# Performance work log

Measured on AMD Instinct MI355X. Metric: run time of the kernel, lower is better.

## Reference

```python
import jax, jax.numpy as jnp
import numpy as np

HEADS = 4
OUT_CH = 32
IN_CH = 128
HC = HEADS * OUT_CH  # 128
N = 100000
G = 1000
E = 1600000
EG = 16000
NEG_SLOPE = 0.2


def gat_conv(x, edge_index, W, att_src, att_dst, bias):
    """PyG-style GATConv (concat heads, self-loops, leaky_relu 0.2, eval mode)."""
    n = x.shape[0]
    loop = jnp.arange(n)
    src = jnp.concatenate([edge_index[0], loop])
    dst = jnp.concatenate([edge_index[1], loop])
    h = (x @ W).reshape(n, HEADS, OUT_CH)            # [n,H,C]
    a_src = (h * att_src).sum(-1)                    # [n,H]
    a_dst = (h * att_dst).sum(-1)                    # [n,H]
    e = jax.nn.leaky_relu(a_src[src] + a_dst[dst], NEG_SLOPE)  # [e,H]
    m = jax.ops.segment_max(e, dst, num_segments=n)
    ex = jnp.exp(e - m[dst])
    s = jax.ops.segment_sum(ex, dst, num_segments=n)
    alpha = ex / (s[dst] + 1e-16)
    out = jax.ops.segment_sum(alpha[:, :, None] * h[src], dst, num_segments=n)
    return out.reshape(n, HC) + bias


def setup_inputs() -> dict:
    key = jax.random.key(0)
    ks = jax.random.split(key, 16)
    inv = 1.0 / np.sqrt(IN_CH)
    invh = 1.0 / np.sqrt(HC)
    return {
        "x": jax.random.normal(ks[0], (N, IN_CH), jnp.float32),
        "x_g": jax.random.normal(ks[1], (G, IN_CH), jnp.float32),
        "edge_index": jax.random.randint(ks[2], (2, E), 0, N, jnp.int32),
        "edge_index_g": jax.random.randint(ks[3], (2, EG), 0, G, jnp.int32),
        "node_group": jax.random.randint(ks[4], (N,), 0, G, jnp.int32),
        "W1": jax.random.normal(ks[5], (IN_CH, HC), jnp.float32) * inv,
        "att_src1": jax.random.normal(ks[6], (HEADS, OUT_CH), jnp.float32) * invh,
        "att_dst1": jax.random.normal(ks[7], (HEADS, OUT_CH), jnp.float32) * invh,
        "bias1": jnp.zeros((HC,), jnp.float32),
        "W2": jax.random.normal(ks[8], (IN_CH, HC), jnp.float32) * inv,
        "att_src2": jax.random.normal(ks[9], (HEADS, OUT_CH), jnp.float32) * invh,
        "att_dst2": jax.random.normal(ks[10], (HEADS, OUT_CH), jnp.float32) * invh,
        "bias2": jnp.zeros((HC,), jnp.float32),
        "W_fc": jax.random.normal(ks[11], (HC, OUT_CH), jnp.float32) * invh,
        "b_fc": jnp.zeros((OUT_CH,), jnp.float32),
    }


def reference(x, x_g, edge_index, edge_index_g, node_group,
              W1, att_src1, att_dst1, bias1,
              W2, att_src2, att_dst2, bias2, W_fc, b_fc):
    x_out = gat_conv(x, edge_index, W1, att_src1, att_dst1, bias1)      # [N,HC]
    x_g_out = gat_conv(x_g, edge_index_g, W2, att_src2, att_dst2, bias2)  # [G,HC]

    # mean of adjacent group features per group (segment mean over group edges)
    adj_sum = jax.ops.segment_sum(x_g_out[edge_index_g[1]], edge_index_g[0], num_segments=G)
    cnt = jax.ops.segment_sum(jnp.ones((edge_index_g.shape[1],), x_g_out.dtype),
                              edge_index_g[0], num_segments=G)
    adj_mean = adj_sum / jnp.maximum(cnt, 1.0)[:, None]                  # [G,HC]

    gf = x_g_out[node_group]          # per-node own-group feature   [N,HC]
    af = adj_mean[node_group]         # per-node adjacent-group mean [N,HC]
    imp_g = jnp.einsum('nc,nc->n', x_out, gf)
    imp_a = jnp.einsum('nc,nc->n', x_out, af)
    upd = x_out + imp_g[:, None] * gf + imp_a[:, None] * af
    out = upd @ W_fc + b_fc
    return out, x_g_out
```

## Files before the change

### kernel.cpp

```cpp
#include <hip/hip_runtime.h>

__host__ __device__ static inline int imin(int a, int b) { return a < b ? a : b; }

__device__ __forceinline__ float lrelu(float v) { return v > 0.f ? v : 0.2f * v; }

__global__ __launch_bounds__(256) void gemm128(const float* __restrict__ X,
                                               const float* __restrict__ W,
                                               const float* __restrict__ att_s,
                                               const float* __restrict__ att_d,
                                               float* __restrict__ H,
                                               float* __restrict__ asrc,
                                               float* __restrict__ adst, int n) {
  __shared__ float Wl[128 * 128];
  __shared__ float Xl[4][4 * 128];
  const int tid = threadIdx.x;
  for (int i = tid; i < 4096; i += 256)
    ((float4*)Wl)[i] = ((const float4*)W)[i];
  __syncthreads();

  const int wave = tid >> 6, lane = tid & 63;
  const float as_l = att_s[lane], as_h = att_s[lane + 64];
  const float ad_l = att_d[lane], ad_h = att_d[lane + 64];
  const int nb = (n + 15) >> 4;
  for (int tb = blockIdx.x; tb < nb; tb += gridDim.x) {
    const int rbase = tb * 16 + wave * 4;
    float2* xl2 = (float2*)&Xl[wave][0];
#pragma unroll
    for (int rr = 0; rr < 4; ++rr) {
      int r = rbase + rr;
      float2 v = make_float2(0.f, 0.f);
      if (r < n) v = ((const float2*)(X + (size_t)r * 128))[lane];
      xl2[rr * 64 + lane] = v;
    }
    float a0[4] = {0, 0, 0, 0}, a1[4] = {0, 0, 0, 0};
#pragma unroll 4
    for (int c = 0; c < 128; ++c) {
      float w0 = Wl[c * 128 + lane];
      float w1 = Wl[c * 128 + lane + 64];
#pragma unroll
      for (int rr = 0; rr < 4; ++rr) {
        float xc = Xl[wave][rr * 128 + c];
        a0[rr] = fmaf(xc, w0, a0[rr]);
        a1[rr] = fmaf(xc, w1, a1[rr]);
      }
    }
#pragma unroll
    for (int rr = 0; rr < 4; ++rr) {
      int r = rbase + rr;
      if (r < n) {
        H[(size_t)r * 128 + lane] = a0[rr];
        H[(size_t)r * 128 + lane + 64] = a1[rr];
        float ps0 = a0[rr] * as_l, pd0 = a0[rr] * ad_l;
        float ps1 = a1[rr] * as_h, pd1 = a1[rr] * ad_h;
#pragma unroll
        for (int m = 16; m >= 1; m >>= 1) {
          ps0 += __shfl_xor(ps0, m);
          pd0 += __shfl_xor(pd0, m);
          ps1 += __shfl_xor(ps1, m);
          pd1 += __shfl_xor(pd1, m);
        }
        if (lane == 0) {
          asrc[(size_t)r * 4 + 0] = ps0;
          adst[(size_t)r * 4 + 0] = pd0;
          asrc[(size_t)r * 4 + 2] = ps1;
          adst[(size_t)r * 4 + 2] = pd1;
        } else if (lane == 32) {
          asrc[(size_t)r * 4 + 1] = ps0;
          adst[(size_t)r * 4 + 1] = pd0;
          asrc[(size_t)r * 4 + 3] = ps1;
          adst[(size_t)r * 4 + 3] = pd1;
        }
      }
    }
  }
}

__global__ __launch_bounds__(256) void count_deg(const int* __restrict__ dst, int ne,
                                                 int* __restrict__ deg) {
  int i = blockIdx.x * 256 + threadIdx.x;
  if (i < ne) atomicAdd(&deg[dst[i]], 1);
}

__global__ __launch_bounds__(256) void scan_part1(const int* __restrict__ in, int n,
                                                  int* __restrict__ bsum) {
  int base = blockIdx.x * 4096 + threadIdx.x * 16;
  int s = 0;
  if (base + 16 <= n) {
    const int4* p = (const int4*)(in + base);
#pragma unroll
    for (int k = 0; k < 4; ++k) {
      int4 v = p[k];
      s += v.x + v.y + v.z + v.w;
    }
  } else {
    for (int k = 0; k < 16; ++k) {
      int i = base + k;
      if (i < n) s += in[i];
    }
  }
#pragma unroll
  for (int o = 1; o < 64; o <<= 1) s += __shfl_xor(s, o);
  __shared__ int ws[4];
  int wave = threadIdx.x >> 6, lane = threadIdx.x & 63;
  if (lane == 0) ws[wave] = s;
  __syncthreads();
  if (threadIdx.x == 0) bsum[blockIdx.x] = ws[0] + ws[1] + ws[2] + ws[3];
}

__global__ __launch_bounds__(256) void scan_part2(int* __restrict__ bsum, int nb,
                                                  int* __restrict__ off, int n) {
  __shared__ int sm[256];
  int tid = threadIdx.x;
  int v = (tid < nb) ? bsum[tid] : 0;
  sm[tid] = v;
  __syncthreads();
  int x = v;
  for (int o = 1; o < 256; o <<= 1) {
    int t = (tid >= o) ? sm[tid - o] : 0;
    __syncthreads();
    x += t;
    sm[tid] = x;
    __syncthreads();
  }
  if (tid < nb) bsum[tid] = x - v;
  if (tid == 0) off[n] = sm[255];
}

__global__ __launch_bounds__(256) void scan_part3(const int* __restrict__ in, int n,
                                                  const int* __restrict__ bsum,
                                                  int* __restrict__ out) {
  int tid = threadIdx.x;
  int base = blockIdx.x * 4096 + tid * 16;
  int vals[16];
  if (base + 16 <= n) {
    const int4* p = (const int4*)(in + base);
#pragma unroll
    for (int k = 0; k < 4; ++k) {
      int4 v = p[k];
      vals[4 * k] = v.x;
      vals[4 * k + 1] = v.y;
      vals[4 * k + 2] = v.z;
      vals[4 * k + 3] = v.w;
    }
  } else {
#pragma unroll
    for (int k = 0; k < 16; ++k) {
      int i = base + k;
      vals[k] = (i < n) ? in[i] : 0;
    }
  }
  int tsum = 0;
#pragma unroll
  for (int k = 0; k < 16; ++k) tsum += vals[k];
  int lane = tid & 63, wave = tid >> 6;
  int inc = tsum;
#pragma unroll
  for (int o = 1; o < 64; o <<= 1) {
    int t = __shfl_up(inc, o);
    if (lane >= o) inc += t;
  }
  int exc = inc - tsum;
  __shared__ int ws[4];
  if (lane == 63) ws[wave] = inc;
  __syncthreads();
  int woff = 0;
  for (int w = 0; w < wave; ++w) woff += ws[w];
  int off0 = bsum[blockIdx.x] + woff + exc;
  int run = 0;
#pragma unroll
  for (int k = 0; k < 16; ++k) {
    int i = base + k;
    if (i < n) out[i] = off0 + run;
    run += vals[k];
  }
}

__global__ __launch_bounds__(256) void fill_csr(const int* __restrict__ src,
                                                const int* __restrict__ dst, int ne,
                                                const int* __restrict__ off,
                                                int* __restrict__ cur,
                                                int* __restrict__ csr) {
  int i = blockIdx.x * 256 + threadIdx.x;
  if (i < ne) {
    int d = dst[i];
    int p = atomicAdd(&cur[d], 1);
    csr[off[d] + p] = src[i];
  }
}

__global__ __launch_bounds__(256) void gat_aggregate(
    const float* __restrict__ H, const float* __restrict__ asrc,
    const float* __restrict__ adst, const int* __restrict__ off,
    const int* __restrict__ csr, const float* __restrict__ bias,
    float* __restrict__ out, int n) {
  __shared__ float4 exl[4][64];
  int gw = (blockIdx.x * 256 + threadIdx.x) >> 6;
  if (gw >= n) return;
  int wave = (threadIdx.x >> 6), lane = threadIdx.x & 63;
  int n0 = off[gw];
  int deg = off[gw + 1] - n0;

  float4 ad = ((const float4*)adst)[gw];
  int c0 = lane * 2;
  int hd = lane >> 4;
  float4 s4 = make_float4(0.f, 0.f, 0.f, 0.f);
  float acc0 = 0.f, acc1 = 0.f;
  const float* exw = (const float*)&exl[wave][0];

  for (int base = 0; base < deg; base += 64) {
    int idx = base + lane;
    bool v = idx < deg;
    int sr = v ? csr[n0 + idx] : 0;
    float4 ex = make_float4(0.f, 0.f, 0.f, 0.f);
    if (v) {
      float4 as = ((const float4*)asrc)[sr];
      ex.x = __expf(lrelu(as.x + ad.x));
      ex.y = __expf(lrelu(as.y + ad.y));
      ex.z = __expf(lrelu(as.z + ad.z));
      ex.w = __expf(lrelu(as.w + ad.w));
      s4.x += ex.x;
      s4.y += ex.y;
      s4.z += ex.z;
      s4.w += ex.w;
    }
    exl[wave][lane] = ex;
    int cnt = imin(64, deg - base);
    for (int j = 0; j < cnt; ++j) {
      int srj = __shfl(sr, j);
      float exh = exw[j * 4 + hd];
      float2 hv = ((const float2*)(H + (size_t)srj * 128))[lane];
      acc0 = fmaf(exh, hv.x, acc0);
      acc1 = fmaf(exh, hv.y, acc1);
    }
  }
#pragma unroll
  for (int o = 1; o < 64; o <<= 1) {
    s4.x += __shfl_xor(s4.x, o);
    s4.y += __shfl_xor(s4.y, o);
    s4.z += __shfl_xor(s4.z, o);
    s4.w += __shfl_xor(s4.w, o);
  }
  float4 asn = ((const float4*)asrc)[gw];
  float4 exs;
  exs.x = __expf(lrelu(asn.x + ad.x));
  exs.y = __expf(lrelu(asn.y + ad.y));
  exs.z = __expf(lrelu(asn.z + ad.z));
  exs.w = __expf(lrelu(asn.w + ad.w));
  s4.x += exs.x;
  s4.y += exs.y;
  s4.z += exs.z;
  s4.w += exs.w;
  float s_h = (hd == 0) ? s4.x : (hd == 1) ? s4.y : (hd == 2) ? s4.z : s4.w;
  float e_h = (hd == 0) ? exs.x : (hd == 1) ? exs.y : (hd == 2) ? exs.z : exs.w;
  float2 hs = ((const float2*)(H + (size_t)gw * 128))[lane];
  acc0 = fmaf(e_h, hs.x, acc0);
  acc1 = fmaf(e_h, hs.y, acc1);
  float inv = 1.f / (s_h + 1e-16f);
  out[(size_t)gw * 128 + c0] = acc0 * inv + bias[c0];
  out[(size_t)gw * 128 + c0 + 1] = acc1 * inv + bias[c0 + 1];
}

__global__ __launch_bounds__(256) void adj_accum(const int* __restrict__ gsrc,
                                                 const int* __restrict__ gdst,
                                                 const float* __restrict__ xgout,
                                                 float* __restrict__ adj,
                                                 float* __restrict__ cnt, int ne) {
  int idx = blockIdx.x * 256 + threadIdx.x;
  if (idx >= ne * 64) return;
  int e = idx >> 6;
  int l = idx & 63;
  int gs = gsrc[e], gd = gdst[e];
  float2 v = ((const float2*)(xgout + (size_t)gd * 128))[l];
  atomicAdd(&adj[(size_t)gs * 128 + 2 * l], v.x);
  atomicAdd(&adj[(size_t)gs * 128 + 2 * l + 1], v.y);
  if (l == 0) atomicAdd(&cnt[gs], 1.0f);
}

__global__ __launch_bounds__(256) void adj_mean_k(float* __restrict__ adj,
                                                  const float* __restrict__ cnt,
                                                  int total) {
  int i = blockIdx.x * 256 + threadIdx.x;
  if (i < total) adj[i] /= fmaxf(cnt[i >> 7], 1.0f);
}

__global__ __launch_bounds__(256) void final_fuse(
    const float* __restrict__ xout, const float* __restrict__ xgout,
    const float* __restrict__ adjm, const int* __restrict__ ngrp,
    const float* __restrict__ Wfc, const float* __restrict__ bfc,
    float* __restrict__ out, int n) {
  __shared__ float Wl[128 * 32];
  __shared__ float up[4][128];
  int tid = threadIdx.x;
  for (int i = tid; i < 1024; i += 256)
    ((float4*)Wl)[i] = ((const float4*)Wfc)[i];
  __syncthreads();

  int wave = tid >> 6, lane = tid & 63;
  int tw = gridDim.x * 4;
  for (int node = blockIdx.x * 4 + wave; node < n; node += tw) {
    int g = ngrp[node];
    float2 xo = ((const float2*)(xout + (size_t)node * 128))[lane];
    float2 gf = ((const float2*)(xgout + (size_t)g * 128))[lane];
    float2 af = ((const float2*)(adjm + (size_t)g * 128))[lane];
    float pg = xo.x * gf.x + xo.y * gf.y;
    float pa = xo.x * af.x + xo.y * af.y;
#pragma unroll
    for (int o = 1; o < 64; o <<= 1) {
      pg += __shfl_xor(pg, o);
      pa += __shfl_xor(pa, o);
    }
    float u0 = xo.x + pg * gf.x + pa * af.x;
    float u1 = xo.y + pg * gf.y + pa * af.y;
    up[wave][lane * 2] = u0;
    up[wave][lane * 2 + 1] = u1;
    int j = lane & 31;
    int ch = (lane >> 5) * 64;
    float acc = 0.f;
#pragma unroll 8
    for (int cc = 0; cc < 64; ++cc)
      acc = fmaf(up[wave][ch + cc], Wl[(ch + cc) * 32 + j], acc);
    acc += __shfl_xor(acc, 32);
    if (lane < 32) out[(size_t)node * 32 + j] = acc + bfc[j];
  }
}

extern "C" void kernel_launch(void* const* d_in, const int* in_sizes, int n_in,
                              void* d_out, int out_size, void* d_ws, size_t ws_size,
                              hipStream_t stream) {
  const float* x = (const float*)d_in[0];
  const float* xg = (const float*)d_in[1];
  const int* ei = (const int*)d_in[2];
  const int* eig = (const int*)d_in[3];
  const int* ngrp = (const int*)d_in[4];
  const float* W1 = (const float*)d_in[5];
  const float* as1 = (const float*)d_in[6];
  const float* ad1 = (const float*)d_in[7];
  const float* b1 = (const float*)d_in[8];
  const float* W2 = (const float*)d_in[9];
  const float* as2 = (const float*)d_in[10];
  const float* ad2 = (const float*)d_in[11];
  const float* b2 = (const float*)d_in[12];
  const float* Wfc = (const float*)d_in[13];
  const float* bfc = (const float*)d_in[14];

  const int N = in_sizes[0] / 128;
  const int G = in_sizes[1] / 128;
  const int E = in_sizes[2] / 2;
  const int EG = in_sizes[3] / 2;

  char* p = (char*)d_ws;
  auto carve = [&](size_t bytes) {
    void* r = (void*)p;
    p += (bytes + 255) & ~(size_t)255;
    return r;
  };
  float* h1 = (float*)carve((size_t)N * 128 * 4);
  float* xout = (float*)carve((size_t)N * 128 * 4);
  float* asrc1 = (float*)carve((size_t)N * 16);
  float* adst1 = (float*)carve((size_t)N * 16);
  int* off1 = (int*)carve((size_t)(N + 1) * 4);
  int* deg1 = (int*)carve((size_t)N * 4);
  int* csr1 = (int*)carve((size_t)E * 4);
  float* h2 = (float*)carve((size_t)G * 128 * 4);
  float* asrc2 = (float*)carve((size_t)G * 16);
  float* adst2 = (float*)carve((size_t)G * 16);
  int* off2 = (int*)carve((size_t)(G + 1) * 4);
  int* deg2 = (int*)carve((size_t)G * 4);
  int* csr2 = (int*)carve((size_t)EG * 4);
  float* adjm = (float*)carve((size_t)G * 128 * 4);
  float* cnt = (float*)carve((size_t)G * 4);
  int* bsum1 = (int*)carve(256 * 4);
  int* bsum2 = (int*)carve(256 * 4);

  float* outN = (float*)d_out;
  float* xgout = (float*)d_out + (size_t)N * 32;

  const int* src1 = ei;
  const int* dst1 = ei + E;
  const int* srcg = eig;
  const int* dstg = eig + EG;

  hipMemsetAsync(deg1, 0, (size_t)N * 4, stream);
  hipMemsetAsync(deg2, 0, (size_t)G * 4, stream);
  hipMemsetAsync(adjm, 0, (size_t)G * 128 * 4, stream);
  hipMemsetAsync(cnt, 0, (size_t)G * 4, stream);

  gemm128<<<imin((N + 15) / 16, 2048), 256, 0, stream>>>(x, W1, as1, ad1, h1, asrc1, adst1, N);
  gemm128<<<imin((G + 15) / 16, 2048), 256, 0, stream>>>(xg, W2, as2, ad2, h2, asrc2, adst2, G);
  count_deg<<<(E + 255) / 256, 256, 0, stream>>>(dst1, E, deg1);
  count_deg<<<(EG + 255) / 256, 256, 0, stream>>>(dstg, EG, deg2);

  const int nb1 = (N + 4095) / 4096;
  const int nb2 = (G + 4095) / 4096;
  scan_part1<<<nb1, 256, 0, stream>>>(deg1, N, bsum1);
  scan_part2<<<1, 256, 0, stream>>>(bsum1, nb1, off1, N);
  scan_part3<<<nb1, 256, 0, stream>>>(deg1, N, bsum1, off1);
  scan_part1<<<nb2, 256, 0, stream>>>(deg2, G, bsum2);
  scan_part2<<<1, 256, 0, stream>>>(bsum2, nb2, off2, G);
  scan_part3<<<nb2, 256, 0, stream>>>(deg2, G, bsum2, off2);

  hipMemsetAsync(deg1, 0, (size_t)N * 4, stream);
  hipMemsetAsync(deg2, 0, (size_t)G * 4, stream);
  fill_csr<<<(E + 255) / 256, 256, 0, stream>>>(src1, dst1, E, off1, deg1, csr1);
  fill_csr<<<(EG + 255) / 256, 256, 0, stream>>>(srcg, dstg, EG, off2, deg2, csr2);
  gat_aggregate<<<(N + 3) / 4, 256, 0, stream>>>(h1, asrc1, adst1, off1, csr1, b1, xout, N);
  gat_aggregate<<<(G + 3) / 4, 256, 0, stream>>>(h2, asrc2, adst2, off2, csr2, b2, xgout, G);
  adj_accum<<<(EG * 64 + 255) / 256, 256, 0, stream>>>(srcg, dstg, xgout, adjm, cnt, EG);
  adj_mean_k<<<(G * 128 + 255) / 256, 256, 0, stream>>>(adjm, cnt, G * 128);
  final_fuse<<<2048, 256, 0, stream>>>(xout, xgout, adjm, ngrp, Wfc, bfc, outN, N);
}
```

Measured before the change: 660.4 us.

## Retile GEMM with transposed swizzled weights, unroll gather loop, fold mean into final

The GEMM kernel now stores W transposed in LDS with an XOR swizzle, reads float4 weight and X vectors, and processes 8 rows per wave instead of 4 (32 rows per block, grid capped at 512). This raises register-level reuse and cuts LDS load instructions per FMA. The aggregation inner loop is unrolled by four so several H row gathers are in flight at once. The separate adj-mean kernel is removed and the division by count moves into final_fuse, saving one launch. Costs are higher register pressure from 16 accumulators per thread plus float4 temporaries, and a per-node reciprocal in final_fuse.

Result: faster. 623.9 us (-5.5%).

```diff
diff --git a/kernel.cpp b/kernel.cpp
--- a/kernel.cpp
+++ b/kernel.cpp
@@ -4,6 +4,7 @@
 
 __device__ __forceinline__ float lrelu(float v) { return v > 0.f ? v : 0.2f * v; }
 
+#define GR 8
 __global__ __launch_bounds__(256) void gemm128(const float* __restrict__ X,
                                                const float* __restrict__ W,
                                                const float* __restrict__ att_s,
@@ -11,41 +12,66 @@
                                                float* __restrict__ H,
                                                float* __restrict__ asrc,
                                                float* __restrict__ adst, int n) {
-  __shared__ float Wl[128 * 128];
-  __shared__ float Xl[4][4 * 128];
+  __shared__ float Wt[128 * 128];
+  __shared__ float Xl[4][GR * 128];
   const int tid = threadIdx.x;
-  for (int i = tid; i < 4096; i += 256)
-    ((float4*)Wl)[i] = ((const float4*)W)[i];
+  for (int i = tid; i < 4096; i += 256) {
+    int c = i >> 5;
+    int j0 = (i & 31) * 4;
+    float4 w = ((const float4*)W)[i];
+    float wv[4] = {w.x, w.y, w.z, w.w};
+    int cu = c >> 2, cr = c & 3;
+#pragma unroll
+    for (int k = 0; k < 4; ++k) {
+      int j = j0 + k;
+      Wt[j * 128 + 4 * (cu ^ (j & 31)) + cr] = wv[k];
+    }
+  }
   __syncthreads();
 
   const int wave = tid >> 6, lane = tid & 63;
   const float as_l = att_s[lane], as_h = att_s[lane + 64];
   const float ad_l = att_d[lane], ad_h = att_d[lane + 64];
-  const int nb = (n + 15) >> 4;
+  const int sw = lane & 31;
+  const float4* wt0 = (const float4*)&Wt[lane * 128];
+  const float4* wt1 = (const float4*)&Wt[(lane + 64) * 128];
+  float* xw = &Xl[wave][0];
+
+  const int nb = (n + 31) >> 5;
   for (int tb = blockIdx.x; tb < nb; tb += gridDim.x) {
-    const int rbase = tb * 16 + wave * 4;
-    float2* xl2 = (float2*)&Xl[wave][0];
-#pragma unroll
-    for (int rr = 0; rr < 4; ++rr) {
+    const int rbase = tb * 32 + wave * GR;
+#pragma unroll
+    for (int rr = 0; rr < GR; ++rr) {
       int r = rbase + rr;
       float2 v = make_float2(0.f, 0.f);
       if (r < n) v = ((const float2*)(X + (size_t)r * 128))[lane];
-      xl2[rr * 64 + lane] = v;
-    }
-    float a0[4] = {0, 0, 0, 0}, a1[4] = {0, 0, 0, 0};
-#pragma unroll 4
-    for (int c = 0; c < 128; ++c) {
-      float w0 = Wl[c * 128 + lane];
-      float w1 = Wl[c * 128 + lane + 64];
-#pragma unroll
-      for (int rr = 0; rr < 4; ++rr) {
-        float xc = Xl[wave][rr * 128 + c];
-        a0[rr] = fmaf(xc, w0, a0[rr]);
-        a1[rr] = fmaf(xc, w1, a1[rr]);
+      ((float2*)(xw + rr * 128))[lane] = v;
+    }
+    float a0[GR], a1[GR];
+#pragma unroll
+    for (int rr = 0; rr < GR; ++rr) {
+      a0[rr] = 0.f;
+      a1[rr] = 0.f;
+    }
+#pragma unroll 2
+    for (int u = 0; u < 32; ++u) {
+      float4 w0 = wt0[u ^ sw];
+      float4 w1 = wt1[u ^ sw];
+#pragma unroll
+      for (int rr = 0; rr < GR; ++rr) {
+        float4 xv = *((const float4*)(xw + rr * 128 + 4 * u));
+        a0[rr] = fmaf(xv.x, w0.x, a0[rr]);
+        a0[rr] = fmaf(xv.y, w0.y, a0[rr]);
+        a0[rr] = fmaf(xv.z, w0.z, a0[rr]);
+        a0[rr] = fmaf(xv.w, w0.w, a0[rr]);
+        a1[rr] = fmaf(xv.x, w1.x, a1[rr]);
+        a1[rr] = fmaf(xv.y, w1.y, a1[rr]);
+        a1[rr] = fmaf(xv.z, w1.z, a1[rr]);
+        a1[rr] = fmaf(xv.w, w1.w, a1[rr]);
       }
     }
 #pragma unroll
-    for (int rr = 0; rr < 4; ++rr) {
+    for (int rr = 0; rr < GR; ++rr) {
       int r = rbase + rr;
       if (r < n) {
         H[(size_t)r * 128 + lane] = a0[rr];
@@ -225,7 +251,30 @@
     }
     exl[wave][lane] = ex;
     int cnt = imin(64, deg - base);
-    for (int j = 0; j < cnt; ++j) {
+    int j = 0;
+    for (; j + 4 <= cnt; j += 4) {
+      int sj0 = __shfl(sr, j);
+      int sj1 = __shfl(sr, j + 1);
+      int sj2 = __shfl(sr, j + 2);
+      int sj3 = __shfl(sr, j + 3);
+      float2 h0 = ((const float2*)(H + (size_t)sj0 * 128))[lane];
+      float2 h1 = ((const float2*)(H + (size_t)sj1 * 128))[lane];
+      float2 h2 = ((const float2*)(H + (size_t)sj2 * 128))[lane];
+      float2 h3 = ((const float2*)(H + (size_t)sj3 * 128))[lane];
+      float e0 = exw[(j + 0) * 4 + hd];
+      float e1 = exw[(j + 1) * 4 + hd];
+      float e2 = exw[(j + 2) * 4 + hd];
+      float e3 = exw[(j + 3) * 4 + hd];
+      acc0 = fmaf(e0, h0.x, acc0);
+      acc1 = fmaf(e0, h0.y, acc1);
+      acc0 = fmaf(e1, h1.x, acc0);
+      acc1 = fmaf(e1, h1.y, acc1);
+      acc0 = fmaf(e2, h2.x, acc0);
+      acc1 = fmaf(e2, h2.y, acc1);
+      acc0 = fmaf(e3, h3.x, acc0);
+      acc1 = fmaf(e3, h3.y, acc1);
+    }
+    for (; j < cnt; ++j) {
       int srj = __shfl(sr, j);
       float exh = exw[j * 4 + hd];
       float2 hv = ((const float2*)(H + (size_t)srj * 128))[lane];
@@ -276,18 +325,11 @@
   if (l == 0) atomicAdd(&cnt[gs], 1.0f);
 }
 
-__global__ __launch_bounds__(256) void adj_mean_k(float* __restrict__ adj,
-                                                  const float* __restrict__ cnt,
-                                                  int total) {
-  int i = blockIdx.x * 256 + threadIdx.x;
-  if (i < total) adj[i] /= fmaxf(cnt[i >> 7], 1.0f);
-}
-
 __global__ __launch_bounds__(256) void final_fuse(
     const float* __restrict__ xout, const float* __restrict__ xgout,
-    const float* __restrict__ adjm, const int* __restrict__ ngrp,
-    const float* __restrict__ Wfc, const float* __restrict__ bfc,
-    float* __restrict__ out, int n) {
+    const float* __restrict__ adjm, const float* __restrict__ cnt,
+    const int* __restrict__ ngrp, const float* __restrict__ Wfc,
+    const float* __restrict__ bfc, float* __restrict__ out, int n) {
   __shared__ float Wl[128 * 32];
   __shared__ float up[4][128];
   int tid = threadIdx.x;
@@ -302,6 +344,9 @@
     float2 xo = ((const float2*)(xout + (size_t)node * 128))[lane];
     float2 gf = ((const float2*)(xgout + (size_t)g * 128))[lane];
     float2 af = ((const float2*)(adjm + (size_t)g * 128))[lane];
+    float cinv = 1.f / fmaxf(cnt[g], 1.0f);
+    af.x *= cinv;
+    af.y *= cinv;
     float pg = xo.x * gf.x + xo.y * gf.y;
     float pa = xo.x * af.x + xo.y * af.y;
 #pragma unroll
@@ -385,8 +430,10 @@
   hipMemsetAsync(adjm, 0, (size_t)G * 128 * 4, stream);
   hipMemsetAsync(cnt, 0, (size_t)G * 4, stream);
 
-  gemm128<<<imin((N + 15) / 16, 2048), 256, 0, stream>>>(x, W1, as1, ad1, h1, asrc1, adst1, N);
-  gemm128<<<imin((G + 15) / 16, 2048), 256, 0, stream>>>(xg, W2, as2, ad2, h2, asrc2, adst2, G);
+  const int nbt1 = (N + 31) / 32;
+  const int nbt2 = (G + 31) / 32;
+  gemm128<<<imin(nbt1, 512), 256, 0, stream>>>(x, W1, as1, ad1, h1, asrc1, adst1, N);
+  gemm128<<<imin(nbt2, 512), 256, 0, stream>>>(xg, W2, as2, ad2, h2, asrc2, adst2, G);
   count_deg<<<(E + 255) / 256, 256, 0, stream>>>(dst1, E, deg1);
   count_deg<<<(EG + 255) / 256, 256, 0, stream>>>(dstg, EG, deg2);
 
@@ -406,6 +453,5 @@
   gat_aggregate<<<(N + 3) / 4, 256, 0, stream>>>(h1, asrc1, adst1, off1, csr1, b1, xout, N);
   gat_aggregate<<<(G + 3) / 4, 256, 0, stream>>>(h2, asrc2, adst2, off2, csr2, b2, xgout, G);
   adj_accum<<<(EG * 64 + 255) / 256, 256, 0, stream>>>(srcg, dstg, xgout, adjm, cnt, EG);
-  adj_mean_k<<<(G * 128 + 255) / 256, 256, 0, stream>>>(adjm, cnt, G * 128);
-  final_fuse<<<2048, 256, 0, stream>>>(xout, xgout, adjm, ngrp, Wfc, bfc, outN, N);
-}
+  final_fuse<<<2048, 256, 0, stream>>>(xout, xgout, adjm, cnt, ngrp, Wfc, bfc, outN, N);
+}
```
